# Optimization experiments

Hardware: AMD Instinct MI355X
Metric: run time of the kernel (lower is better)

Reference implementation:

```python
import jax, jax.numpy as jnp
import numpy as np

E, H, I, T, K = 8, 2048, 768, 1024, 2


def setup_inputs() -> dict:
    key = jax.random.key(0)
    k1, k2, k3, k4, k5 = jax.random.split(key, 5)
    hidden_states = jax.random.normal(k1, (T, H), jnp.float32)
    routing_weights = jax.random.uniform(k2, (T, K), jnp.float32)
    selected_experts = jax.random.randint(k3, (T, K), 0, E, jnp.int32)
    gate_up_proj = jax.random.normal(k4, (E, H, 2 * I), jnp.float32) * 0.02
    down_proj = jax.random.normal(k5, (E, I, H), jnp.float32) * 0.02
    return {
        "hidden_states": hidden_states,
        "routing_weights": routing_weights,
        "gate_up_proj": gate_up_proj,
        "down_proj": down_proj,
        "selected_experts": selected_experts,
    }


def _grouped_gemm(x, w, expert_ids):
    # x: [N, k], w: [E, k, d], expert_ids: [N] (sorted by expert).
    # Dense-masked grouped GEMM: accumulate each expert's masked matmul.
    n = x.shape[0]
    acc0 = jnp.zeros((n, w.shape[-1]), x.dtype)

    def step(acc, ew):
        e, we = ew
        xm = jnp.where((expert_ids == e)[:, None], x, jnp.zeros((), x.dtype))
        return acc + xm @ we, None

    acc, _ = jax.lax.scan(step, acc0, (jnp.arange(w.shape[0]), w))
    return acc


def reference(hidden_states, routing_weights, gate_up_proj, down_proj, selected_experts):
    t, h = hidden_states.shape
    k = selected_experts.shape[1]
    flat = selected_experts.reshape(-1)                     # [T*K]
    sort_idx = jnp.argsort(flat)                            # stable sort by expert id (permute)
    token_idx = sort_idx // k                               # source token per permuted row
    permuted = hidden_states[token_idx]                     # [T*K, H]
    experts_sorted = flat[sort_idx]                         # [T*K]

    fc1 = _grouped_gemm(permuted, gate_up_proj, experts_sorted)   # [T*K, 2I]
    a, b = jnp.split(fc1, 2, axis=-1)
    act = jax.nn.silu(a) * b                                # npu_swiglu
    fc2 = _grouped_gemm(act, down_proj, experts_sorted)     # [T*K, H]

    inv = jnp.argsort(sort_idx)                             # unpermute map (row_ids_map)
    unperm = fc2[inv].reshape(t, k, h)                      # [T, K, H]
    return jnp.einsum('tkh,tk->th', unperm, routing_weights)
```

## Files before the change

### kernel.cpp

```cpp
#include <hip/hip_runtime.h>
#include <math.h>

#define E_  8
#define H_  2048
#define I_  768
#define T_  1024
#define K_  2
#define TK_ 2048
#define GU_ 1536

typedef __bf16 bf16x8 __attribute__((ext_vector_type(8)));
typedef float  f32x4  __attribute__((ext_vector_type(4)));

static __device__ __forceinline__ short f2bf(float f) {
  union { float f; unsigned u; } v; v.f = f;
  unsigned r = (v.u + 0x7fffu + ((v.u >> 16) & 1u)) >> 16;
  return (short)r;
}

static __device__ __forceinline__ unsigned pk2bf(float a, float b) {
  unsigned ua = __float_as_uint(a) + 0x8000u;
  unsigned ub = __float_as_uint(b) + 0x8000u;
  return __builtin_amdgcn_perm(ub, ua, 0x07060302u);
}

#define GLOAD_LDS16(g, l)                                                   \
  __builtin_amdgcn_global_load_lds(                                         \
      (const __attribute__((address_space(1))) void*)(g),                   \
      (__attribute__((address_space(3))) void*)(l), 16, 0, 0)

#define MFMA_BF16_16x16x32 __builtin_amdgcn_mfma_f32_16x16x32_bf16

static __device__ __forceinline__ bf16x8 frag_ld(const unsigned short* base,
                                                 int row, int oct) {
  return *(const bf16x8*)(base + row * 64 + ((oct ^ (row & 7)) * 8));
}

#define STEP(IT, VC, VN)                                                    \
  do {                                                                      \
    asm volatile("s_waitcnt vmcnt(4)" ::: "memory");                        \
    __builtin_amdgcn_s_barrier();                                           \
    __builtin_amdgcn_sched_barrier(0);                                      \
    int k1_ = ((IT) + 1 < niter ? (IT) + 1 : niter - 1) * 64;               \
    int k2_ = ((IT) + 2 < niter ? (IT) + 2 : niter - 1) * 64;               \
    issueA(cur ^ 1, k1_);                                                   \
    __builtin_amdgcn_sched_barrier(0);                                      \
    loadB(VN, k2_);                                                         \
    const unsigned short* a_ = &As[cur][0];                                 \
    const unsigned short* b_ = &Bs[cur][0];                                 \
    _Pragma("unroll")                                                       \
    for (int kk = 0; kk < 2; ++kk) {                                        \
      int o = kk * 4 + qf;                                                  \
      bf16x8 af0 = frag_ld(a_, w * 32 + m,      o);                         \
      bf16x8 af1 = frag_ld(a_, w * 32 + 16 + m, o);                         \
      bf16x8 b0  = frag_ld(b_, m,      o);                                  \
      bf16x8 b1  = frag_ld(b_, 16 + m, o);                                  \
      bf16x8 b2  = frag_ld(b_, 32 + m, o);                                  \
      bf16x8 b3  = frag_ld(b_, 48 + m, o);                                  \
      acc[0][0] = MFMA_BF16_16x16x32(af0, b0, acc[0][0], 0, 0, 0);          \
      acc[0][1] = MFMA_BF16_16x16x32(af0, b1, acc[0][1], 0, 0, 0);          \
      acc[0][2] = MFMA_BF16_16x16x32(af0, b2, acc[0][2], 0, 0, 0);          \
      acc[0][3] = MFMA_BF16_16x16x32(af0, b3, acc[0][3], 0, 0, 0);          \
      acc[1][0] = MFMA_BF16_16x16x32(af1, b0, acc[1][0], 0, 0, 0);          \
      acc[1][1] = MFMA_BF16_16x16x32(af1, b1, acc[1][1], 0, 0, 0);          \
      acc[1][2] = MFMA_BF16_16x16x32(af1, b2, acc[1][2], 0, 0, 0);          \
      acc[1][3] = MFMA_BF16_16x16x32(af1, b3, acc[1][3], 0, 0, 0);          \
    }                                                                       \
    writeB(cur ^ 1, VC);                                                    \
    asm volatile("s_waitcnt lgkmcnt(0)" ::: "memory");                      \
    __builtin_amdgcn_sched_barrier(0);                                      \
    cur ^= 1;                                                               \
  } while (0)

__global__ __launch_bounds__(256) void prep_kernel(
    const float* __restrict__ X, unsigned short* __restrict__ Xb,
    float* __restrict__ out,
    const int* __restrict__ sel, int* __restrict__ offs,
    int* __restrict__ rows) {
  __shared__ int cnt[E_], cur[E_], loff[E_ + 1];
  if (blockIdx.x < 2048) {
    int i = blockIdx.x * 256 + threadIdx.x;
    float4 v = ((const float4*)X)[i];
    unsigned p0 = pk2bf(v.x, v.y), p1 = pk2bf(v.z, v.w);
    ((uint2*)Xb)[i] = make_uint2(p0, p1);
    ((float4*)out)[i] = make_float4(0.f, 0.f, 0.f, 0.f);
    return;
  }
  int t = threadIdx.x;
  if (t < E_) { cnt[t] = 0; cur[t] = 0; }
  __syncthreads();
  for (int p = t; p < TK_; p += 256) atomicAdd(&cnt[sel[p]], 1);
  __syncthreads();
  if (t == 0) {
    int s = 0;
    for (int e = 0; e < E_; ++e) { loff[e] = s; s += cnt[e]; }
    loff[E_] = s;
  }
  __syncthreads();
  if (t <= E_) offs[t] = loff[t];
  for (int p = t; p < TK_; p += 256) {
    int e = sel[p];
    int pos = loff[e] + atomicAdd(&cur[e], 1);
    rows[pos] = p;
  }
}

__global__ __launch_bounds__(256, 3) void fc1_mfma(
    const unsigned short* __restrict__ Xb, const float* __restrict__ GUP,
    const int* __restrict__ offs, const int* __restrict__ rows,
    unsigned short* __restrict__ act) {
  __shared__ __align__(16) unsigned short As[2][128 * 64];
  __shared__ __align__(16) unsigned short Bs[2][64 * 64];

  int e    = blockIdx.y >> 4;
  int rbeg = offs[e], rend = offs[e + 1];
  int row0 = rbeg + (blockIdx.y & 15) * 128;
  if (row0 >= rend) return;
  int c0 = blockIdx.x * 32;

  int tid = threadIdx.x, lane = tid & 63, w = tid >> 6;
  int rl  = lane >> 3;
  int oct = (lane & 7) ^ rl;

  const unsigned short* agp[4];
#pragma unroll
  for (int i = 0; i < 4; ++i) {
    int arow = row0 + w * 32 + i * 8 + rl;
    int aidx = arow < rend ? arow : rend - 1;
    agp[i] = Xb + (size_t)(rows[aidx] >> 1) * H_ + oct * 8;
  }
  auto issueA = [&](int buf, int k0) {
#pragma unroll
    for (int i = 0; i < 4; ++i)
      GLOAD_LDS16(agp[i] + k0, &As[buf][0] + (w * 32 + i * 8) * 64);
  };

  int kt = tid >> 4, nt = tid & 15;
  int gbase = (nt < 8) ? (c0 + nt * 4) : (I_ + c0 + (nt - 8) * 4);
  const float* gupe = GUP + (size_t)e * H_ * GU_ + gbase;

  auto loadB = [&](float4 (&vb)[4], int k0) {
#pragma unroll
    for (int i = 0; i < 4; ++i)
      vb[i] = *(const float4*)(gupe + (size_t)(k0 + kt * 4 + i) * GU_);
  };
  auto writeB = [&](int buf, const float4 (&vb)[4]) {
#pragma unroll
    for (int j = 0; j < 4; ++j) {
      int n = nt * 4 + j;
      unsigned u0 = pk2bf(((const float*)&vb[0])[j], ((const float*)&vb[1])[j]);
      unsigned u1 = pk2bf(((const float*)&vb[2])[j], ((const float*)&vb[3])[j]);
      int phys = (kt >> 1) ^ (n & 7);
      *(uint2*)(&Bs[buf][0] + n * 64 + phys * 8 + (kt & 1) * 4) =
          make_uint2(u0, u1);
    }
  };

  int m = lane & 15, qf = lane >> 4;
  f32x4 acc[2][4] = {};
  float4 vbA[4], vbB[4];

  issueA(0, 0);
  __builtin_amdgcn_sched_barrier(0);
  loadB(vbB, 0);
  writeB(0, vbB);
  loadB(vbA, 64);
  asm volatile("s_waitcnt lgkmcnt(0)" ::: "memory");
  __builtin_amdgcn_sched_barrier(0);

  const int niter = H_ / 64;
  int cur = 0;
#pragma unroll 1
  for (int it = 0; it < niter; it += 2) {
    STEP(it,     vbA, vbB);
    STEP(it + 1, vbB, vbA);
  }

#pragma unroll
  for (int mt = 0; mt < 2; ++mt)
#pragma unroll
    for (int g = 0; g < 2; ++g)
#pragma unroll
      for (int r = 0; r < 4; ++r) {
        int prow = row0 + w * 32 + mt * 16 + qf * 4 + r;
        if (prow < rend) {
          float gv = acc[mt][g][r], uv = acc[mt][g + 2][r];
          float a = gv / (1.0f + __expf(-gv)) * uv;
          act[(size_t)prow * I_ + c0 + g * 16 + m] = (unsigned short)f2bf(a);
        }
      }
}

__global__ __launch_bounds__(256, 3) void fc2_mfma(
    const unsigned short* __restrict__ act, const float* __restrict__ DWN,
    const float* __restrict__ RW,
    const int* __restrict__ offs, const int* __restrict__ rows,
    float* __restrict__ out) {
  __shared__ __align__(16) unsigned short As[2][128 * 64];
  __shared__ __align__(16) unsigned short Bs[2][64 * 64];

  int e    = blockIdx.y >> 4;
  int rbeg = offs[e], rend = offs[e + 1];
  int row0 = rbeg + (blockIdx.y & 15) * 128;
  if (row0 >= rend) return;
  int c0 = blockIdx.x * 64;

  int tid = threadIdx.x, lane = tid & 63, w = tid >> 6;
  int rl  = lane >> 3;
  int oct = (lane & 7) ^ rl;

  const unsigned short* agp[4];
#pragma unroll
  for (int i = 0; i < 4; ++i) {
    int arow = row0 + w * 32 + i * 8 + rl;
    int aidx = arow < rend ? arow : rend - 1;
    agp[i] = act + (size_t)aidx * I_ + oct * 8;
  }
  auto issueA = [&](int buf, int k0) {
#pragma unroll
    for (int i = 0; i < 4; ++i)
      GLOAD_LDS16(agp[i] + k0, &As[buf][0] + (w * 32 + i * 8) * 64);
  };

  int kt = tid >> 4, nt = tid & 15;
  const float* dwe = DWN + (size_t)e * I_ * H_ + c0 + nt * 4;

  auto loadB = [&](float4 (&vb)[4], int k0) {
#pragma unroll
    for (int i = 0; i < 4; ++i)
      vb[i] = *(const float4*)(dwe + (size_t)(k0 + kt * 4 + i) * H_);
  };
  auto writeB = [&](int buf, const float4 (&vb)[4]) {
#pragma unroll
    for (int j = 0; j < 4; ++j) {
      int n = nt * 4 + j;
      unsigned u0 = pk2bf(((const float*)&vb[0])[j], ((const float*)&vb[1])[j]);
      unsigned u1 = pk2bf(((const float*)&vb[2])[j], ((const float*)&vb[3])[j]);
      int phys = (kt >> 1) ^ (n & 7);
      *(uint2*)(&Bs[buf][0] + n * 64 + phys * 8 + (kt & 1) * 4) =
          make_uint2(u0, u1);
    }
  };

  int m = lane & 15, qf = lane >> 4;
  f32x4 acc[2][4] = {};
  float4 vbA[4], vbB[4];

  issueA(0, 0);
  __builtin_amdgcn_sched_barrier(0);
  loadB(vbB, 0);
  writeB(0, vbB);
  loadB(vbA, 64);
  asm volatile("s_waitcnt lgkmcnt(0)" ::: "memory");
  __builtin_amdgcn_sched_barrier(0);

  const int niter = I_ / 64;
  int cur = 0;
#pragma unroll 1
  for (int it = 0; it < niter; it += 2) {
    STEP(it,     vbA, vbB);
    STEP(it + 1, vbB, vbA);
  }

#pragma unroll
  for (int mt = 0; mt < 2; ++mt)
#pragma unroll
    for (int r = 0; r < 4; ++r) {
      int prow = row0 + w * 32 + mt * 16 + qf * 4 + r;
      if (prow < rend) {
        int pair = rows[prow];
        float rw = RW[pair];
        float* orow = out + (size_t)(pair >> 1) * H_ + c0 + m;
#pragma unroll
        for (int ntile = 0; ntile < 4; ++ntile)
          atomicAdd(orow + ntile * 16, rw * acc[mt][ntile][r]);
      }
    }
}

extern "C" void kernel_launch(void* const* d_in, const int* in_sizes, int n_in,
                              void* d_out, int out_size, void* d_ws, size_t ws_size,
                              hipStream_t stream) {
  const float* X   = (const float*)d_in[0];
  const float* RW  = (const float*)d_in[1];
  const float* GUP = (const float*)d_in[2];
  const float* DWN = (const float*)d_in[3];
  const int*   SEL = (const int*)d_in[4];
  float* out = (float*)d_out;

  char* ws = (char*)d_ws;
  int* offs = (int*)ws;
  int* rows = (int*)(ws + 1024);
  unsigned short* Xb  = (unsigned short*)(ws + 16384);
  unsigned short* act = (unsigned short*)(ws + 16384 + 4194304);

  hipLaunchKernelGGL(prep_kernel, dim3(2049), dim3(256), 0, stream,
                     X, Xb, out, SEL, offs, rows);
  hipLaunchKernelGGL(fc1_mfma, dim3(24, 128), dim3(256), 0, stream,
                     Xb, GUP, offs, rows, act);
  hipLaunchKernelGGL(fc2_mfma, dim3(32, 128), dim3(256), 0, stream,
                     act, DWN, RW, offs, rows, out);
}
```

Before: 253.8 us.

## Deepen B prefetch, reswizzle B LDS, and replace atomic scatter with staged combine

```diff
diff --git a/kernel.cpp b/kernel.cpp
--- a/kernel.cpp
+++ b/kernel.cpp
@@ -36,27 +36,33 @@
   return *(const bf16x8*)(base + row * 64 + ((oct ^ (row & 7)) * 8));
 }
 
-#define STEP(IT, VC, VN)                                                    \
+static __device__ __forceinline__ bf16x8 bfrag_ld(const unsigned short* base,
+                                                  int n, int o) {
+  int phys = (o ^ (n & 7) ^ (n >> 3)) & 7;
+  return *(const bf16x8*)(base + n * 64 + phys * 8);
+}
+
+#define STEP(IT, G)                                                         \
   do {                                                                      \
     asm volatile("s_waitcnt vmcnt(4)" ::: "memory");                        \
     __builtin_amdgcn_s_barrier();                                           \
     __builtin_amdgcn_sched_barrier(0);                                      \
     int k1_ = ((IT) + 1 < niter ? (IT) + 1 : niter - 1) * 64;               \
-    int k2_ = ((IT) + 2 < niter ? (IT) + 2 : niter - 1) * 64;               \
+    int k3_ = ((IT) + 3 < niter ? (IT) + 3 : niter - 1) * 64;               \
     issueA(cur ^ 1, k1_);                                                   \
     __builtin_amdgcn_sched_barrier(0);                                      \
-    loadB(VN, k2_);                                                         \
     const unsigned short* a_ = &As[cur][0];                                 \
     const unsigned short* b_ = &Bs[cur][0];                                 \
+    __builtin_amdgcn_s_setprio(1);                                          \
     _Pragma("unroll")                                                       \
     for (int kk = 0; kk < 2; ++kk) {                                        \
       int o = kk * 4 + qf;                                                  \
       bf16x8 af0 = frag_ld(a_, w * 32 + m,      o);                         \
       bf16x8 af1 = frag_ld(a_, w * 32 + 16 + m, o);                         \
-      bf16x8 b0  = frag_ld(b_, m,      o);                                  \
-      bf16x8 b1  = frag_ld(b_, 16 + m, o);                                  \
-      bf16x8 b2  = frag_ld(b_, 32 + m, o);                                  \
-      bf16x8 b3  = frag_ld(b_, 48 + m, o);                                  \
+      bf16x8 b0  = bfrag_ld(b_, m,      o);                                 \
+      bf16x8 b1  = bfrag_ld(b_, 16 + m, o);                                 \
+      bf16x8 b2  = bfrag_ld(b_, 32 + m, o);                                 \
+      bf16x8 b3  = bfrag_ld(b_, 48 + m, o);                                 \
       acc[0][0] = MFMA_BF16_16x16x32(af0, b0, acc[0][0], 0, 0, 0);          \
       acc[0][1] = MFMA_BF16_16x16x32(af0, b1, acc[0][1], 0, 0, 0);          \
       acc[0][2] = MFMA_BF16_16x16x32(af0, b2, acc[0][2], 0, 0, 0);          \
@@ -66,7 +72,9 @@
       acc[1][2] = MFMA_BF16_16x16x32(af1, b2, acc[1][2], 0, 0, 0);          \
       acc[1][3] = MFMA_BF16_16x16x32(af1, b3, acc[1][3], 0, 0, 0);          \
     }                                                                       \
-    writeB(cur ^ 1, VC);                                                    \
+    __builtin_amdgcn_s_setprio(0);                                          \
+    writeB(cur ^ 1, G);                                                     \
+    loadB(G, k3_);                                                          \
     asm volatile("s_waitcnt lgkmcnt(0)" ::: "memory");                      \
     __builtin_amdgcn_sched_barrier(0);                                      \
     cur ^= 1;                                                               \
@@ -76,14 +84,14 @@
     const float* __restrict__ X, unsigned short* __restrict__ Xb,
     float* __restrict__ out,
     const int* __restrict__ sel, int* __restrict__ offs,
-    int* __restrict__ rows) {
+    int* __restrict__ rows, int* __restrict__ inv, int zero_out) {
   __shared__ int cnt[E_], cur[E_], loff[E_ + 1];
   if (blockIdx.x < 2048) {
     int i = blockIdx.x * 256 + threadIdx.x;
     float4 v = ((const float4*)X)[i];
     unsigned p0 = pk2bf(v.x, v.y), p1 = pk2bf(v.z, v.w);
     ((uint2*)Xb)[i] = make_uint2(p0, p1);
-    ((float4*)out)[i] = make_float4(0.f, 0.f, 0.f, 0.f);
+    if (zero_out) ((float4*)out)[i] = make_float4(0.f, 0.f, 0.f, 0.f);
     return;
   }
   int t = threadIdx.x;
@@ -102,6 +110,7 @@
     int e = sel[p];
     int pos = loff[e] + atomicAdd(&cur[e], 1);
     rows[pos] = p;
+    inv[p] = pos;
   }
 }
 
@@ -150,7 +159,7 @@
       int n = nt * 4 + j;
       unsigned u0 = pk2bf(((const float*)&vb[0])[j], ((const float*)&vb[1])[j]);
       unsigned u1 = pk2bf(((const float*)&vb[2])[j], ((const float*)&vb[3])[j]);
-      int phys = (kt >> 1) ^ (n & 7);
+      int phys = ((kt >> 1) ^ (n & 7) ^ (n >> 3)) & 7;
       *(uint2*)(&Bs[buf][0] + n * 64 + phys * 8 + (kt & 1) * 4) =
           make_uint2(u0, u1);
     }
@@ -162,9 +171,10 @@
 
   issueA(0, 0);
   __builtin_amdgcn_sched_barrier(0);
-  loadB(vbB, 0);
-  writeB(0, vbB);
+  loadB(vbA, 0);
+  writeB(0, vbA);
   loadB(vbA, 64);
+  loadB(vbB, 128);
   asm volatile("s_waitcnt lgkmcnt(0)" ::: "memory");
   __builtin_amdgcn_sched_barrier(0);
 
@@ -172,9 +182,10 @@
   int cur = 0;
 #pragma unroll 1
   for (int it = 0; it < niter; it += 2) {
-    STEP(it,     vbA, vbB);
-    STEP(it + 1, vbB, vbA);
-  }
+    STEP(it,     vbA);
+    STEP(it + 1, vbB);
+  }
+  asm volatile("s_waitcnt vmcnt(0)" ::: "memory");
 
 #pragma unroll
   for (int mt = 0; mt < 2; ++mt)
@@ -195,7 +206,7 @@
     const unsigned short* __restrict__ act, const float* __restrict__ DWN,
     const float* __restrict__ RW,
     const int* __restrict__ offs, const int* __restrict__ rows,
-    float* __restrict__ out) {
+    float* __restrict__ stage, float* __restrict__ out, int use_stage) {
   __shared__ __align__(16) unsigned short As[2][128 * 64];
   __shared__ __align__(16) unsigned short Bs[2][64 * 64];
 
@@ -236,7 +247,7 @@
       int n = nt * 4 + j;
       unsigned u0 = pk2bf(((const float*)&vb[0])[j], ((const float*)&vb[1])[j]);
       unsigned u1 = pk2bf(((const float*)&vb[2])[j], ((const float*)&vb[3])[j]);
-      int phys = (kt >> 1) ^ (n & 7);
+      int phys = ((kt >> 1) ^ (n & 7) ^ (n >> 3)) & 7;
       *(uint2*)(&Bs[buf][0] + n * 64 + phys * 8 + (kt & 1) * 4) =
           make_uint2(u0, u1);
     }
@@ -248,9 +259,10 @@
 
   issueA(0, 0);
   __builtin_amdgcn_sched_barrier(0);
-  loadB(vbB, 0);
-  writeB(0, vbB);
+  loadB(vbA, 0);
+  writeB(0, vbA);
   loadB(vbA, 64);
+  loadB(vbB, 128);
   asm volatile("s_waitcnt lgkmcnt(0)" ::: "memory");
   __builtin_amdgcn_sched_barrier(0);
 
@@ -258,9 +270,10 @@
   int cur = 0;
 #pragma unroll 1
   for (int it = 0; it < niter; it += 2) {
-    STEP(it,     vbA, vbB);
-    STEP(it + 1, vbB, vbA);
-  }
+    STEP(it,     vbA);
+    STEP(it + 1, vbB);
+  }
+  asm volatile("s_waitcnt vmcnt(0)" ::: "memory");
 
 #pragma unroll
   for (int mt = 0; mt < 2; ++mt)
@@ -270,12 +283,32 @@
       if (prow < rend) {
         int pair = rows[prow];
         float rw = RW[pair];
-        float* orow = out + (size_t)(pair >> 1) * H_ + c0 + m;
-#pragma unroll
-        for (int ntile = 0; ntile < 4; ++ntile)
-          atomicAdd(orow + ntile * 16, rw * acc[mt][ntile][r]);
+        if (use_stage) {
+          float* srow = stage + (size_t)prow * H_ + c0 + m;
+          srow[0]  = rw * acc[mt][0][r];
+          srow[16] = rw * acc[mt][1][r];
+          srow[32] = rw * acc[mt][2][r];
+          srow[48] = rw * acc[mt][3][r];
+        } else {
+          float* orow = out + (size_t)(pair >> 1) * H_ + c0 + m;
+#pragma unroll
+          for (int ntile = 0; ntile < 4; ++ntile)
+            atomicAdd(orow + ntile * 16, rw * acc[mt][ntile][r]);
+        }
       }
     }
+}
+
+__global__ __launch_bounds__(256) void combine_kernel(
+    const float* __restrict__ stage, const int* __restrict__ inv,
+    float* __restrict__ out) {
+  int idx = blockIdx.x * 256 + threadIdx.x;
+  int t  = idx >> 9;
+  int q  = idx & 511;
+  int2 pp = *(const int2*)(inv + 2 * t);
+  float4 a = ((const float4*)(stage + (size_t)pp.x * H_))[q];
+  float4 b = ((const float4*)(stage + (size_t)pp.y * H_))[q];
+  ((float4*)out)[idx] = make_float4(a.x + b.x, a.y + b.y, a.z + b.z, a.w + b.w);
 }
 
 extern "C" void kernel_launch(void* const* d_in, const int* in_sizes, int n_in,
@@ -291,13 +324,32 @@
   char* ws = (char*)d_ws;
   int* offs = (int*)ws;
   int* rows = (int*)(ws + 1024);
-  unsigned short* Xb  = (unsigned short*)(ws + 16384);
-  unsigned short* act = (unsigned short*)(ws + 16384 + 4194304);
+  int* inv  = (int*)(ws + 16384);
+
+  const size_t stage_bytes = (size_t)TK_ * H_ * 4;
+  const size_t act_bytes   = (size_t)TK_ * I_ * 2;
+  const size_t need_stage  = 32768 + stage_bytes + act_bytes;
+
+  int use_stage = (ws_size >= need_stage) ? 1 : 0;
+  unsigned short *Xb, *act;
+  float* stage;
+  if (use_stage) {
+    stage = (float*)(ws + 32768);
+    Xb    = (unsigned short*)(ws + 32768);
+    act   = (unsigned short*)(ws + 32768 + stage_bytes);
+  } else {
+    stage = (float*)(ws + 32768);
+    Xb    = (unsigned short*)(ws + 32768);
+    act   = (unsigned short*)(ws + 32768 + 4194304);
+  }
 
   hipLaunchKernelGGL(prep_kernel, dim3(2049), dim3(256), 0, stream,
-                     X, Xb, out, SEL, offs, rows);
+                     X, Xb, out, SEL, offs, rows, inv, use_stage ? 0 : 1);
   hipLaunchKernelGGL(fc1_mfma, dim3(24, 128), dim3(256), 0, stream,
                      Xb, GUP, offs, rows, act);
   hipLaunchKernelGGL(fc2_mfma, dim3(32, 128), dim3(256), 0, stream,
-                     act, DWN, RW, offs, rows, out);
-}
+                     act, DWN, RW, offs, rows, stage, out, use_stage);
+  if (use_stage)
+    hipLaunchKernelGGL(combine_kernel, dim3(2048), dim3(256), 0, stream,
+                       stage, inv, out);
+}
```

Measured after the change: 251.1 us. Within noise of the previous version (-1.1%).
